# Kernel tuning notes

Hardware: AMD Instinct MI355X
Metric: run time of the kernel (lower is better)

Reference implementation:

```python
import jax, jax.numpy as jnp
import numpy as np

N = 20000   # nodes
E = 320000  # edges (avg degree 16)
H = 4       # heads
C = 128     # per-head / output channels (concat=False -> mean over heads)
IN = 2      # init_channels (TSP coords)
NEG_SLOPE = 0.2


def setup_inputs() -> dict:
    key = jax.random.key(0)
    ks = jax.random.split(key, 32)
    s = 0.1
    def W(k, shape):
        return (jax.random.normal(k, shape, jnp.float32) * s)
    inp = {
        "x": jax.random.normal(ks[0], (N, IN), jnp.float32),
        "edge_index": jax.random.randint(ks[1], (2, E), 0, N, jnp.int32),
        "edge_attr": jax.random.uniform(ks[2], (E, 1), jnp.float32),
    }
    i = 3
    for b in range(2):  # two parallel GATBlocks
        inp[f"Wsrc{b}"]  = W(ks[i+0], (IN, H * C))
        inp[f"bsrc{b}"]  = jnp.zeros((H * C,), jnp.float32)
        inp[f"Wdst{b}"]  = W(ks[i+1], (IN, H * C))
        inp[f"bdst{b}"]  = jnp.zeros((H * C,), jnp.float32)
        inp[f"Wedge{b}"] = W(ks[i+2], (1, H * C))
        inp[f"att{b}"]   = W(ks[i+3], (H, C))
        inp[f"bias{b}"]  = jnp.zeros((C,), jnp.float32)
        inp[f"Wres{b}"]  = W(ks[i+4], (IN, C))  # SkipConnection projection (2 -> 128)
        i += 5
    inp["Wfuse"] = W(ks[i], (2 * C, C))
    inp["bfuse"] = jnp.zeros((C,), jnp.float32)
    return inp


def _gat_block(x, src, dst, ea, Wsrc, bsrc, Wdst, bdst, Wedge, att, bias, Wres):
    # GATv2Conv (concat=False) + ReLU + residual projection
    xs = (x @ Wsrc + bsrc).reshape(N, H, C)   # lin_l (source / message)
    xd = (x @ Wdst + bdst).reshape(N, H, C)   # lin_r (target)
    ee = (ea @ Wedge).reshape(-1, H, C)       # lin_edge
    e = jax.nn.leaky_relu(xs[src] + xd[dst] + ee, NEG_SLOPE)  # [Etot,H,C]
    logits = jnp.einsum('ehc,hc->eh', e, att)                 # [Etot,H]
    # segment softmax over incoming edges of each target node
    m = jax.ops.segment_max(logits, dst, num_segments=N)
    m = jnp.where(jnp.isfinite(m), m, 0.0)
    p = jnp.exp(logits - m[dst])
    denom = jax.ops.segment_sum(p, dst, num_segments=N)
    alpha = p / (denom[dst] + 1e-16)                          # [Etot,H]
    agg = jax.ops.segment_sum(xs[src] * alpha[:, :, None], dst, num_segments=N)
    out = agg.mean(axis=1) + bias                             # concat=False: mean heads
    return jax.nn.relu(out) + x @ Wres                        # ReLU then skip add


def reference(x, edge_index, edge_attr,
              Wsrc0, bsrc0, Wdst0, bdst0, Wedge0, att0, bias0, Wres0,
              Wsrc1, bsrc1, Wdst1, bdst1, Wedge1, att1, bias1, Wres1,
              Wfuse, bfuse):
    src, dst = edge_index[0], edge_index[1]
    # PyG default add_self_loops=True, fill_value='mean' for edge_attr
    loop = jnp.arange(N, dtype=src.dtype)
    src_a = jnp.concatenate([src, loop])
    dst_a = jnp.concatenate([dst, loop])
    mean_attr = jnp.mean(edge_attr, axis=0, keepdims=True)
    ea = jnp.concatenate([edge_attr, jnp.broadcast_to(mean_attr, (N, 1))], axis=0)

    h0 = _gat_block(x, src_a, dst_a, ea, Wsrc0, bsrc0, Wdst0, bdst0, Wedge0, att0, bias0, Wres0)
    h1 = _gat_block(x, src_a, dst_a, ea, Wsrc1, bsrc1, Wdst1, bdst1, Wedge1, att1, bias1, Wres1)
    xc = jnp.concatenate([h0, h1], axis=-1)       # [N, 2C]
    return jax.nn.relu(xc @ Wfuse + bfuse)        # [N, C]
```

## Files before the change

### kernel.cpp

```cpp
#include <hip/hip_runtime.h>

#define HH 4
#define CC 128
#define NPB 64

typedef __attribute__((ext_vector_type(8))) short short8v;
typedef __attribute__((ext_vector_type(4))) float f32x4;

static inline size_t roundup256(size_t x) { return (x + 255) & ~(size_t)255; }

static __device__ __forceinline__ unsigned short f2bf(float f) {
    unsigned int u = __float_as_uint(f);
    unsigned int r = (u + 0x7FFFu + ((u >> 16) & 1u)) >> 16;
    return (unsigned short)r;
}

__global__ __launch_bounds__(256) void prep_kernel(
    const int* __restrict__ ei, const float* __restrict__ eattr,
    float* __restrict__ meansum, float* __restrict__ Lin, int* __restrict__ cnt,
    const float* __restrict__ Wsrc0, const float* __restrict__ bsrc0,
    const float* __restrict__ Wdst0, const float* __restrict__ bdst0,
    const float* __restrict__ Wedge0, const float* __restrict__ att0,
    const float* __restrict__ Wsrc1, const float* __restrict__ bsrc1,
    const float* __restrict__ Wdst1, const float* __restrict__ bdst1,
    const float* __restrict__ Wedge1, const float* __restrict__ att1,
    const float* __restrict__ Wfuse,
    float* __restrict__ packed, unsigned short* __restrict__ pwB, int E)
{
    int tid = blockIdx.x * 256 + threadIdx.x;
    int lane = threadIdx.x & 63, wid = threadIdx.x >> 6;
    float s = 0.f;
    if (tid < E) {
        atomicAdd(&cnt[ei[E + tid]], 1);
        s = eattr[tid];
    }
    #pragma unroll
    for (int off = 32; off > 0; off >>= 1) s += __shfl_down(s, off, 64);
    __shared__ float wsum[4];
    if (lane == 0) wsum[wid] = s;
    __syncthreads();
    if (threadIdx.x == 0)
        atomicAdd(meansum, wsum[0] + wsum[1] + wsum[2] + wsum[3]);

    if (blockIdx.x < 4) {
        int b = tid >> 9;
        int hc = tid & 511;
        int c = hc & 127;
        int h = hc >> 7;
        int bh = b * 4 + h;
        const float* Ws = b ? Wsrc1 : Wsrc0;
        const float* bs = b ? bsrc1 : bsrc0;
        const float* Wd = b ? Wdst1 : Wdst0;
        const float* bd = b ? bdst1 : bdst0;
        const float* We = b ? Wedge1 : Wedge0;
        const float* at = b ? att1 : att0;
        float A = Ws[hc], B = Ws[512 + hc];
        float C = Wd[hc], D = Wd[512 + hc];
        float Ec = We[hc];
        float F = bs[hc] + bd[hc];
        float a = at[hc];
        float4* r = (float4*)(packed + ((size_t)(bh * 128 + c)) * 8);
        r[0] = make_float4(A, B, C, D);
        r[1] = make_float4(Ec, F, 0.4f * a, 0.f);
        float sa = 0.6f * a;
        float vals[6] = {sa * A, sa * B, sa * C, sa * D, sa * Ec, sa * F};
        #pragma unroll
        for (int k = 0; k < 6; ++k) {
            float v = vals[k];
            #pragma unroll
            for (int off = 32; off > 0; off >>= 1) v += __shfl_down(v, off, 64);
            vals[k] = v;
        }
        __shared__ float Ls[4][6];
        if (lane == 0) {
            #pragma unroll
            for (int k = 0; k < 6; ++k) Ls[wid][k] = vals[k];
        }
        __syncthreads();
        if (threadIdx.x < 12) {
            int w2 = threadIdx.x / 6;
            int k = threadIdx.x % 6;
            int bhg = blockIdx.x * 2 + w2;
            Lin[bhg * 6 + k] = Ls[w2 * 2][k] + Ls[w2 * 2 + 1][k];
        }
    }

    if (blockIdx.x < 16) {
        int ct = tid >> 9;
        int kc = (tid >> 6) & 7;
        int l  = tid & 63;
        int c = ct * 16 + (l & 15);
        int kb = kc * 32 + (l >> 4) * 8;
        unsigned short v[8];
        #pragma unroll
        for (int j = 0; j < 8; ++j)
            v[j] = f2bf(Wfuse[(kb + j) * CC + c]);
        unsigned short* dst = pwB + (size_t)tid * 8;
        #pragma unroll
        for (int j = 0; j < 8; ++j) dst[j] = v[j];
    }
}

__global__ __launch_bounds__(1024) void scan_kernel(const int* __restrict__ cnt,
                                                    int* __restrict__ rowptr,
                                                    int* __restrict__ cur, int N) {
    const int CH = 32;
    int t = threadIdx.x;
    int base = t * CH;
    int local[CH];
    int s = 0;
    #pragma unroll
    for (int i = 0; i < CH; ++i) {
        int idx = base + i;
        int v = (idx < N) ? cnt[idx] + 1 : 0;
        local[i] = s;
        s += v;
    }
    __shared__ int sums[1024];
    sums[t] = s;
    __syncthreads();
    for (int off = 1; off < 1024; off <<= 1) {
        int v = (t >= off) ? sums[t - off] : 0;
        __syncthreads();
        sums[t] += v;
        __syncthreads();
    }
    int excl = sums[t] - s;
    #pragma unroll
    for (int i = 0; i < CH; ++i) {
        int idx = base + i;
        if (idx < N) {
            int v = excl + local[i];
            rowptr[idx] = v;
            cur[idx] = v;
        }
    }
    if (t == 1023) rowptr[N] = excl + s;
}

__global__ __launch_bounds__(256) void scatter_kernel(
    const int* __restrict__ ei, const float* __restrict__ x,
    const float* __restrict__ eattr, const float* __restrict__ meansum,
    int* __restrict__ cur, float4* __restrict__ ed4, float* __restrict__ ea1,
    int N, int E) {
    int e = blockIdx.x * 256 + threadIdx.x;
    int Etot = E + N;
    if (e >= Etot) return;
    int src, dst;
    float ea;
    if (e < E) { src = ei[e]; dst = ei[E + e]; ea = eattr[e]; }
    else       { src = e - E; dst = src; ea = meansum[0] / (float)E; }
    int pos = atomicAdd(&cur[dst], 1);
    const float2* x2 = (const float2*)x;
    float2 xs = x2[src];
    float2 xd = x2[dst];
    ed4[pos] = make_float4(xs.x, xs.y, xd.x, xd.y);
    ea1[pos] = ea;
}

__global__ __launch_bounds__(256) void logits_kernel(
    const float4* __restrict__ ed4,
    const float* __restrict__ ea1,
    const float* __restrict__ Lin,
    const float4* __restrict__ pw,
    float* __restrict__ p8, int EtotPad, int nchunks)
{
    int blk = blockIdx.x;
    int bh = blk / nchunks;
    int chunk = blk - bh * nchunks;
    int t = threadIdx.x;
    int iA = chunk * 512 + t;
    int iB = iA + 256;
    float4 eA = ed4[iA], eB = ed4[iB];
    float aA = ea1[iA], aB = ea1[iB];

    const float4* wp = pw + (size_t)bh * 256;
    float a0 = 0.f, a1 = 0.f;
    #pragma unroll 8
    for (int c = 0; c < 128; ++c) {
        float4 w0 = wp[2 * c];
        float4 w1 = wp[2 * c + 1];
        float uA = fmaf(w0.x, eA.x,
                   fmaf(w0.y, eA.y,
                   fmaf(w0.z, eA.z,
                   fmaf(w0.w, eA.w,
                   fmaf(w1.x, aA, w1.y)))));
        float uB = fmaf(w0.x, eB.x,
                   fmaf(w0.y, eB.y,
                   fmaf(w0.z, eB.z,
                   fmaf(w0.w, eB.w,
                   fmaf(w1.x, aB, w1.y)))));
        a0 = fmaf(w1.z, __builtin_fabsf(uA), a0);
        a1 = fmaf(w1.z, __builtin_fabsf(uB), a1);
    }

    const float* Lp = Lin + bh * 6;
    float lgA = fmaf(Lp[0], eA.x, fmaf(Lp[1], eA.y, fmaf(Lp[2], eA.z,
                fmaf(Lp[3], eA.w, fmaf(Lp[4], aA, Lp[5]))))) + a0;
    float lgB = fmaf(Lp[0], eB.x, fmaf(Lp[1], eB.y, fmaf(Lp[2], eB.z,
                fmaf(Lp[3], eB.w, fmaf(Lp[4], aB, Lp[5]))))) + a1;
    float* plane = p8 + (size_t)bh * EtotPad;
    plane[iA] = __expf(lgA);
    plane[iB] = __expf(lgB);
}

__global__ __launch_bounds__(256) void nodeS_kernel(
    const int* __restrict__ rowptr, const float4* __restrict__ ed4,
    const float* __restrict__ p8, float* __restrict__ S, int N, int EtotPad)
{
    int t = threadIdx.x;
    int g = t >> 3, bh = t & 7;
    int n = blockIdx.x * 32 + g;
    if (n >= N) return;
    int beg = rowptr[n], end = rowptr[n + 1];
    const float* plane = p8 + (size_t)bh * EtotPad;
    float s0 = 0.f, s1 = 0.f, sb = 0.f;
    for (int i = beg; i < end; ++i) {
        float4 ed = ed4[i];
        float p = plane[i];
        s0 = fmaf(p, ed.x, s0);
        s1 = fmaf(p, ed.y, s1);
        sb += p;
    }
    float rin = 1.f / (sb + 1e-16f);
    float* Sp = S + (size_t)n * 24 + bh * 3;
    Sp[0] = s0 * rin;
    Sp[1] = s1 * rin;
    Sp[2] = sb * rin;
}

__global__ __launch_bounds__(512) void node_kernel(
    const float* __restrict__ x,
    const float* __restrict__ S,
    const float* __restrict__ Wsrc0, const float* __restrict__ bsrc0,
    const float* __restrict__ bias0, const float* __restrict__ Wres0,
    const float* __restrict__ Wsrc1, const float* __restrict__ bsrc1,
    const float* __restrict__ bias1, const float* __restrict__ Wres1,
    const unsigned short* __restrict__ pwB, const float* __restrict__ bfuse,
    float* __restrict__ out, int N)
{
    __shared__ __align__(16) unsigned short hb[NPB][264];
    int t = threadIdx.x;
    int c = t & (CC - 1);
    int quarter = t >> 7;
    int n0 = blockIdx.x * NPB;

    float w00[HH], w01[HH], wb0[HH], w10[HH], w11[HH], wb1[HH];
    #pragma unroll
    for (int h = 0; h < HH; ++h) {
        w00[h] = Wsrc0[h * CC + c];
        w01[h] = Wsrc0[512 + h * CC + c];
        wb0[h] = bsrc0[h * CC + c];
        w10[h] = Wsrc1[h * CC + c];
        w11[h] = Wsrc1[512 + h * CC + c];
        wb1[h] = bsrc1[h * CC + c];
    }
    float bi0 = bias0[c], bi1 = bias1[c];
    float r00 = Wres0[c], r01 = Wres0[CC + c];
    float r10 = Wres1[c], r11 = Wres1[CC + c];

    for (int ni = quarter; ni < NPB; ni += 4) {
        int n = n0 + ni;
        if (n < N) {
            float x0 = x[2 * n], x1 = x[2 * n + 1];
            const float4* Sp4 = (const float4*)(S + (size_t)n * 24);
            float4 q0 = Sp4[0], q1 = Sp4[1], q2 = Sp4[2];
            float4 q3 = Sp4[3], q4 = Sp4[4], q5 = Sp4[5];
            float h0v, h1v;
            {
                float s0[HH] = {q0.x, q0.w, q1.z, q2.y};
                float s1[HH] = {q0.y, q1.x, q1.w, q2.z};
                float sb[HH] = {q0.z, q1.y, q2.x, q2.w};
                float acc = 0.f;
                #pragma unroll
                for (int h = 0; h < HH; ++h)
                    acc += fmaf(w00[h], s0[h], fmaf(w01[h], s1[h], wb0[h] * sb[h]));
                float o = fmaxf(acc * 0.25f + bi0, 0.f);
                h0v = o + x0 * r00 + x1 * r01;
            }
            {
                float s0[HH] = {q3.x, q3.w, q4.z, q5.y};
                float s1[HH] = {q3.y, q4.x, q4.w, q5.z};
                float sb[HH] = {q3.z, q4.y, q5.x, q5.w};
                float acc = 0.f;
                #pragma unroll
                for (int h = 0; h < HH; ++h)
                    acc += fmaf(w10[h], s0[h], fmaf(w11[h], s1[h], wb1[h] * sb[h]));
                float o = fmaxf(acc * 0.25f + bi1, 0.f);
                h1v = o + x0 * r10 + x1 * r11;
            }
            hb[ni][c] = f2bf(h0v);
            hb[ni][CC + c] = f2bf(h1v);
        }
    }
    __syncthreads();

    int w = t >> 6;
    int l = t & 63;
    int nt = w & 3;
    int cthalf = w >> 2;
    int row = nt * 16 + (l & 15);

    short8v a[8];
    #pragma unroll
    for (int kc = 0; kc < 8; ++kc)
        a[kc] = *reinterpret_cast<const short8v*>(&hb[row][kc * 32 + (l >> 4) * 8]);

    const short8v* pB = reinterpret_cast<const short8v*>(pwB);
    #pragma unroll
    for (int ci = 0; ci < 4; ++ci) {
        int ct = cthalf * 4 + ci;
        f32x4 acc = {0.f, 0.f, 0.f, 0.f};
        #pragma unroll
        for (int kc = 0; kc < 8; ++kc) {
            short8v b = pB[(ct * 8 + kc) * 64 + l];
            acc = __builtin_amdgcn_mfma_f32_16x16x32_bf16(a[kc], b, acc, 0, 0, 0);
        }
        int ch = ct * 16 + (l & 15);
        float bi = bfuse[ch];
        #pragma unroll
        for (int j = 0; j < 4; ++j) {
            int n = n0 + nt * 16 + (l >> 4) * 4 + j;
            if (n < N) out[(size_t)n * CC + ch] = fmaxf(acc[j] + bi, 0.f);
        }
    }
}

extern "C" void kernel_launch(void* const* d_in, const int* in_sizes, int n_in,
                              void* d_out, int out_size, void* d_ws, size_t ws_size,
                              hipStream_t stream) {
    const float* x      = (const float*)d_in[0];
    const int*   ei     = (const int*)d_in[1];
    const float* eattr  = (const float*)d_in[2];
    const float* Wsrc0  = (const float*)d_in[3];
    const float* bsrc0  = (const float*)d_in[4];
    const float* Wdst0  = (const float*)d_in[5];
    const float* bdst0  = (const float*)d_in[6];
    const float* Wedge0 = (const float*)d_in[7];
    const float* att0   = (const float*)d_in[8];
    const float* bias0  = (const float*)d_in[9];
    const float* Wres0  = (const float*)d_in[10];
    const float* Wsrc1  = (const float*)d_in[11];
    const float* bsrc1  = (const float*)d_in[12];
    const float* Wdst1  = (const float*)d_in[13];
    const float* bdst1  = (const float*)d_in[14];
    const float* Wedge1 = (const float*)d_in[15];
    const float* att1   = (const float*)d_in[16];
    const float* bias1  = (const float*)d_in[17];
    const float* Wres1  = (const float*)d_in[18];
    const float* Wfuse  = (const float*)d_in[19];
    const float* bfuse  = (const float*)d_in[20];
    float* out = (float*)d_out;

    int N = in_sizes[0] / 2;
    int E = in_sizes[1] / 2;
    int Etot = E + N;
    int EtotPad = (Etot + 511) & ~511;

    size_t off = 0;
    float* meansum = (float*)((char*)d_ws + off);  off += 256;
    int*   cnt     = (int*)((char*)d_ws + off);    off += roundup256((size_t)N * sizeof(int));
    size_t zero_bytes = off;
    float* Lin     = (float*)((char*)d_ws + off);  off += 256;
    int*   cur     = (int*)((char*)d_ws + off);    off += roundup256((size_t)N * sizeof(int));
    int*   rowptr  = (int*)((char*)d_ws + off);    off += roundup256((size_t)(N + 1) * sizeof(int));
    float* packed  = (float*)((char*)d_ws + off);  off += roundup256(8 * 128 * 8 * sizeof(float));
    unsigned short* pwB = (unsigned short*)((char*)d_ws + off);
                                                   off += roundup256(8 * 8 * 64 * 8 * sizeof(unsigned short));
    float4* ed4    = (float4*)((char*)d_ws + off); off += roundup256((size_t)EtotPad * sizeof(float4));
    float* ea1     = (float*)((char*)d_ws + off);  off += roundup256((size_t)EtotPad * sizeof(float));
    float* p8      = (float*)((char*)d_ws + off);  off += roundup256((size_t)EtotPad * 8 * sizeof(float));
    float* S       = (float*)((char*)d_ws + off);  off += roundup256((size_t)24 * N * sizeof(float));

    hipMemsetAsync(d_ws, 0, zero_bytes, stream);

    prep_kernel<<<(E + 255) / 256, 256, 0, stream>>>(
        ei, eattr, meansum, Lin, cnt,
        Wsrc0, bsrc0, Wdst0, bdst0, Wedge0, att0,
        Wsrc1, bsrc1, Wdst1, bdst1, Wedge1, att1,
        Wfuse, packed, pwB, E);

    scan_kernel<<<1, 1024, 0, stream>>>(cnt, rowptr, cur, N);

    scatter_kernel<<<(Etot + 255) / 256, 256, 0, stream>>>(
        ei, x, eattr, meansum, cur, ed4, ea1, N, E);

    int nchunks = EtotPad / 512;
    logits_kernel<<<8 * nchunks, 256, 0, stream>>>(
        ed4, ea1, Lin, (const float4*)packed, p8, EtotPad, nchunks);

    nodeS_kernel<<<(N + 31) / 32, 256, 0, stream>>>(rowptr, ed4, p8, S, N, EtotPad);

    node_kernel<<<(N + NPB - 1) / NPB, 512, 0, stream>>>(
        x, S,
        Wsrc0, bsrc0, bias0, Wres0,
        Wsrc1, bsrc1, bias1, Wres1,
        pwB, bfuse, out, N);
}
```

Baseline: 170.0 us.

## Compute GATv2 edge logits with bf16 MFMA instead of scalar FMA loops

The per-edge, per-channel pre-activation (a linear map of source/target coords, edge attribute and bias) is now a bf16 MFMA 16x16x32 product. Edge features form the A fragment and packed per-head weights form the B fragment. The abs-weighted reduction over channels uses cross-lane shuffles, and each block handles all 8 block-heads for 256 edges instead of one head per block. This targets the scalar FMA cost of the logits kernel. It adds bf16 rounding of the coordinates and weights, which may shift attention logits slightly.

```diff
diff --git a/kernel.cpp b/kernel.cpp
--- a/kernel.cpp
+++ b/kernel.cpp
@@ -17,7 +17,8 @@
 
 __global__ __launch_bounds__(256) void prep_kernel(
     const int* __restrict__ ei, const float* __restrict__ eattr,
-    float* __restrict__ meansum, float* __restrict__ Lin, int* __restrict__ cnt,
+    float* __restrict__ meansum, float* __restrict__ Lin,
+    float* __restrict__ gtab, int* __restrict__ cnt,
     const float* __restrict__ Wsrc0, const float* __restrict__ bsrc0,
     const float* __restrict__ Wdst0, const float* __restrict__ bdst0,
     const float* __restrict__ Wedge0, const float* __restrict__ att0,
@@ -25,7 +26,7 @@
     const float* __restrict__ Wdst1, const float* __restrict__ bdst1,
     const float* __restrict__ Wedge1, const float* __restrict__ att1,
     const float* __restrict__ Wfuse,
-    float* __restrict__ packed, unsigned short* __restrict__ pwB, int E)
+    unsigned short* __restrict__ pwL, unsigned short* __restrict__ pwB, int E)
 {
     int tid = blockIdx.x * 256 + threadIdx.x;
     int lane = threadIdx.x & 63, wid = threadIdx.x >> 6;
@@ -59,9 +60,7 @@
         float Ec = We[hc];
         float F = bs[hc] + bd[hc];
         float a = at[hc];
-        float4* r = (float4*)(packed + ((size_t)(bh * 128 + c)) * 8);
-        r[0] = make_float4(A, B, C, D);
-        r[1] = make_float4(Ec, F, 0.4f * a, 0.f);
+        gtab[bh * 128 + c] = 0.4f * a;
         float sa = 0.6f * a;
         float vals[6] = {sa * A, sa * B, sa * C, sa * D, sa * Ec, sa * F};
         #pragma unroll
@@ -85,17 +84,45 @@
         }
     }
 
-    if (blockIdx.x < 16) {
-        int ct = tid >> 9;
-        int kc = (tid >> 6) & 7;
-        int l  = tid & 63;
+    if (blockIdx.x >= 4 && blockIdx.x < 20) {
+        int t2 = tid - 1024;
+        int ct = t2 >> 9;
+        int kc = (t2 >> 6) & 7;
+        int l  = t2 & 63;
         int c = ct * 16 + (l & 15);
         int kb = kc * 32 + (l >> 4) * 8;
         unsigned short v[8];
         #pragma unroll
         for (int j = 0; j < 8; ++j)
             v[j] = f2bf(Wfuse[(kb + j) * CC + c]);
-        unsigned short* dst = pwB + (size_t)tid * 8;
+        unsigned short* dst = pwB + (size_t)t2 * 8;
+        #pragma unroll
+        for (int j = 0; j < 8; ++j) dst[j] = v[j];
+    }
+
+    if (blockIdx.x >= 20 && blockIdx.x < 36) {
+        int t2 = tid - 5120;
+        int bh = t2 >> 9;
+        int ct = (t2 >> 6) & 7;
+        int l  = t2 & 63;
+        unsigned short v[8] = {0, 0, 0, 0, 0, 0, 0, 0};
+        if (l < 16) {
+            int b = bh >> 2, h = bh & 3;
+            int c = ct * 16 + l;
+            int hc = h * 128 + c;
+            const float* Ws = b ? Wsrc1 : Wsrc0;
+            const float* bs = b ? bsrc1 : bsrc0;
+            const float* Wd = b ? Wdst1 : Wdst0;
+            const float* bd = b ? bdst1 : bdst0;
+            const float* We = b ? Wedge1 : Wedge0;
+            v[0] = f2bf(Ws[hc]);
+            v[1] = f2bf(Ws[512 + hc]);
+            v[2] = f2bf(Wd[hc]);
+            v[3] = f2bf(Wd[512 + hc]);
+            v[4] = f2bf(We[hc]);
+            v[5] = f2bf(bs[hc] + bd[hc]);
+        }
+        unsigned short* dst = pwL + (size_t)t2 * 8;
         #pragma unroll
         for (int j = 0; j < 8; ++j) dst[j] = v[j];
     }
@@ -162,46 +189,80 @@
     const float4* __restrict__ ed4,
     const float* __restrict__ ea1,
     const float* __restrict__ Lin,
-    const float4* __restrict__ pw,
-    float* __restrict__ p8, int EtotPad, int nchunks)
+    const float* __restrict__ gtab,
+    const unsigned short* __restrict__ pwL,
+    float* __restrict__ p8, int EtotPad)
 {
-    int blk = blockIdx.x;
-    int bh = blk / nchunks;
-    int chunk = blk - bh * nchunks;
     int t = threadIdx.x;
-    int iA = chunk * 512 + t;
-    int iB = iA + 256;
-    float4 eA = ed4[iA], eB = ed4[iB];
-    float aA = ea1[iA], aB = ea1[iB];
-
-    const float4* wp = pw + (size_t)bh * 256;
-    float a0 = 0.f, a1 = 0.f;
-    #pragma unroll 8
-    for (int c = 0; c < 128; ++c) {
-        float4 w0 = wp[2 * c];
-        float4 w1 = wp[2 * c + 1];
-        float uA = fmaf(w0.x, eA.x,
-                   fmaf(w0.y, eA.y,
-                   fmaf(w0.z, eA.z,
-                   fmaf(w0.w, eA.w,
-                   fmaf(w1.x, aA, w1.y)))));
-        float uB = fmaf(w0.x, eB.x,
-                   fmaf(w0.y, eB.y,
-                   fmaf(w0.z, eB.z,
-                   fmaf(w0.w, eB.w,
-                   fmaf(w1.x, aB, w1.y)))));
-        a0 = fmaf(w1.z, __builtin_fabsf(uA), a0);
-        a1 = fmaf(w1.z, __builtin_fabsf(uB), a1);
-    }
-
-    const float* Lp = Lin + bh * 6;
-    float lgA = fmaf(Lp[0], eA.x, fmaf(Lp[1], eA.y, fmaf(Lp[2], eA.z,
-                fmaf(Lp[3], eA.w, fmaf(Lp[4], aA, Lp[5]))))) + a0;
-    float lgB = fmaf(Lp[0], eB.x, fmaf(Lp[1], eB.y, fmaf(Lp[2], eB.z,
-                fmaf(Lp[3], eB.w, fmaf(Lp[4], aB, Lp[5]))))) + a1;
-    float* plane = p8 + (size_t)bh * EtotPad;
-    plane[iA] = __expf(lgA);
-    plane[iB] = __expf(lgB);
+    int w = t >> 6, l = t & 63;
+    int base = blockIdx.x * 256 + w * 64;
+    int col = l & 15, grp = l >> 4;
+
+    short8v a[4];
+    #pragma unroll
+    for (int et = 0; et < 4; ++et) {
+        short8v v = {0, 0, 0, 0, 0, 0, 0, 0};
+        if (grp == 0) {
+            int e = base + et * 16 + col;
+            float4 ev = ed4[e];
+            float ea = ea1[e];
+            v[0] = (short)f2bf(ev.x);
+            v[1] = (short)f2bf(ev.y);
+            v[2] = (short)f2bf(ev.z);
+            v[3] = (short)f2bf(ev.w);
+            v[4] = (short)f2bf(ea);
+            v[5] = (short)f2bf(1.0f);
+        }
+        a[et] = v;
+    }
+
+    const short8v* pB = reinterpret_cast<const short8v*>(pwL);
+
+    #pragma unroll
+    for (int bh = 0; bh < 8; ++bh) {
+        f32x4 acc[4];
+        #pragma unroll
+        for (int et = 0; et < 4; ++et) acc[et] = (f32x4){0.f, 0.f, 0.f, 0.f};
+
+        #pragma unroll
+        for (int ct = 0; ct < 8; ++ct) {
+            short8v bfrag = pB[(bh * 8 + ct) * 64 + l];
+            float g = gtab[bh * 128 + ct * 16 + col];
+            #pragma unroll
+            for (int et = 0; et < 4; ++et) {
+                f32x4 u = __builtin_amdgcn_mfma_f32_16x16x32_bf16(
+                    a[et], bfrag, (f32x4){0.f, 0.f, 0.f, 0.f}, 0, 0, 0);
+                #pragma unroll
+                for (int j = 0; j < 4; ++j)
+                    acc[et][j] = fmaf(g, __builtin_fabsf(u[j]), acc[et][j]);
+            }
+        }
+
+        const float* Lp = Lin + bh * 6;
+        float l0 = Lp[0], l1 = Lp[1], l2 = Lp[2], l3 = Lp[3], l4 = Lp[4], l5 = Lp[5];
+        float* plane = p8 + (size_t)bh * EtotPad;
+
+        #pragma unroll
+        for (int et = 0; et < 4; ++et) {
+            float s0 = acc[et][0], s1 = acc[et][1], s2 = acc[et][2], s3 = acc[et][3];
+            #pragma unroll
+            for (int m = 1; m < 16; m <<= 1) {
+                s0 += __shfl_xor(s0, m);
+                s1 += __shfl_xor(s1, m);
+                s2 += __shfl_xor(s2, m);
+                s3 += __shfl_xor(s3, m);
+            }
+            if (col < 4) {
+                float sv = (col == 0) ? s0 : (col == 1) ? s1 : (col == 2) ? s2 : s3;
+                int e = base + et * 16 + grp * 4 + col;
+                float4 ev = ed4[e];
+                float ea = ea1[e];
+                float lg = fmaf(l0, ev.x, fmaf(l1, ev.y, fmaf(l2, ev.z,
+                           fmaf(l3, ev.w, fmaf(l4, ea, l5))))) + sv;
+                plane[e] = __expf(lg);
+            }
+        }
+    }
 }
 
 __global__ __launch_bounds__(256) void nodeS_kernel(
@@ -362,11 +423,13 @@
     int*   cnt     = (int*)((char*)d_ws + off);    off += roundup256((size_t)N * sizeof(int));
     size_t zero_bytes = off;
     float* Lin     = (float*)((char*)d_ws + off);  off += 256;
+    float* gtab    = (float*)((char*)d_ws + off);  off += roundup256(1024 * sizeof(float));
     int*   cur     = (int*)((char*)d_ws + off);    off += roundup256((size_t)N * sizeof(int));
     int*   rowptr  = (int*)((char*)d_ws + off);    off += roundup256((size_t)(N + 1) * sizeof(int));
-    float* packed  = (float*)((char*)d_ws + off);  off += roundup256(8 * 128 * 8 * sizeof(float));
     unsigned short* pwB = (unsigned short*)((char*)d_ws + off);
-                                                   off += roundup256(8 * 8 * 64 * 8 * sizeof(unsigned short));
+                                                   off += roundup256(4096 * 8 * sizeof(unsigned short));
+    unsigned short* pwL = (unsigned short*)((char*)d_ws + off);
+                                                   off += roundup256(4096 * 8 * sizeof(unsigned short));
     float4* ed4    = (float4*)((char*)d_ws + off); off += roundup256((size_t)EtotPad * sizeof(float4));
     float* ea1     = (float*)((char*)d_ws + off);  off += roundup256((size_t)EtotPad * sizeof(float));
     float* p8      = (float*)((char*)d_ws + off);  off += roundup256((size_t)EtotPad * 8 * sizeof(float));
@@ -375,19 +438,18 @@
     hipMemsetAsync(d_ws, 0, zero_bytes, stream);
 
     prep_kernel<<<(E + 255) / 256, 256, 0, stream>>>(
-        ei, eattr, meansum, Lin, cnt,
+        ei, eattr, meansum, Lin, gtab, cnt,
         Wsrc0, bsrc0, Wdst0, bdst0, Wedge0, att0,
         Wsrc1, bsrc1, Wdst1, bdst1, Wedge1, att1,
-        Wfuse, packed, pwB, E);
+        Wfuse, pwL, pwB, E);
 
     scan_kernel<<<1, 1024, 0, stream>>>(cnt, rowptr, cur, N);
 
     scatter_kernel<<<(Etot + 255) / 256, 256, 0, stream>>>(
         ei, x, eattr, meansum, cur, ed4, ea1, N, E);
 
-    int nchunks = EtotPad / 512;
-    logits_kernel<<<8 * nchunks, 256, 0, stream>>>(
-        ed4, ea1, Lin, (const float4*)packed, p8, EtotPad, nchunks);
+    logits_kernel<<<EtotPad / 256, 256, 0, stream>>>(
+        ed4, ea1, Lin, gtab, pwL, p8, EtotPad);
 
     nodeS_kernel<<<(N + 31) / 32, 256, 0, stream>>>(rowptr, ed4, p8, S, N, EtotPad);
 
```

Result: slower. 198.7 us (+16.9%).

## Fuse per-node softmax aggregation into node kernel via shared memory

Applied to the files above, without the earlier changes.

Removes the separate nodeS kernel and computes the per-node normalized attention sums inside node_kernel, keeping them in shared memory instead of writing and rereading a global S buffer. The scatter kernel now also stores the source index per CSR slot, and the aggregation gathers x[src] through it rather than reading the 16-byte ed4 records. It also moves the Wfuse bf16 packing to prep blocks 4–19 so it no longer shares blocks 0–3 with other prep work. The cost is an extra esrc write and random gathers into x, plus a longer, possibly imbalanced prologue in node_kernel before its barrier.

```diff
diff --git a/kernel.cpp b/kernel.cpp
--- a/kernel.cpp
+++ b/kernel.cpp
@@ -85,17 +85,18 @@
         }
     }
 
-    if (blockIdx.x < 16) {
-        int ct = tid >> 9;
-        int kc = (tid >> 6) & 7;
-        int l  = tid & 63;
+    if (blockIdx.x >= 4 && blockIdx.x < 20) {
+        int t2 = tid - 1024;
+        int ct = t2 >> 9;
+        int kc = (t2 >> 6) & 7;
+        int l  = t2 & 63;
         int c = ct * 16 + (l & 15);
         int kb = kc * 32 + (l >> 4) * 8;
         unsigned short v[8];
         #pragma unroll
         for (int j = 0; j < 8; ++j)
             v[j] = f2bf(Wfuse[(kb + j) * CC + c]);
-        unsigned short* dst = pwB + (size_t)tid * 8;
+        unsigned short* dst = pwB + (size_t)t2 * 8;
         #pragma unroll
         for (int j = 0; j < 8; ++j) dst[j] = v[j];
     }
@@ -142,7 +143,7 @@
     const int* __restrict__ ei, const float* __restrict__ x,
     const float* __restrict__ eattr, const float* __restrict__ meansum,
     int* __restrict__ cur, float4* __restrict__ ed4, float* __restrict__ ea1,
-    int N, int E) {
+    int* __restrict__ esrc, int N, int E) {
     int e = blockIdx.x * 256 + threadIdx.x;
     int Etot = E + N;
     if (e >= Etot) return;
@@ -156,6 +157,7 @@
     float2 xd = x2[dst];
     ed4[pos] = make_float4(xs.x, xs.y, xd.x, xd.y);
     ea1[pos] = ea;
+    esrc[pos] = src;
 }
 
 __global__ __launch_bounds__(256) void logits_kernel(
@@ -204,46 +206,49 @@
     plane[iB] = __expf(lgB);
 }
 
-__global__ __launch_bounds__(256) void nodeS_kernel(
-    const int* __restrict__ rowptr, const float4* __restrict__ ed4,
-    const float* __restrict__ p8, float* __restrict__ S, int N, int EtotPad)
-{
-    int t = threadIdx.x;
-    int g = t >> 3, bh = t & 7;
-    int n = blockIdx.x * 32 + g;
-    if (n >= N) return;
-    int beg = rowptr[n], end = rowptr[n + 1];
-    const float* plane = p8 + (size_t)bh * EtotPad;
-    float s0 = 0.f, s1 = 0.f, sb = 0.f;
-    for (int i = beg; i < end; ++i) {
-        float4 ed = ed4[i];
-        float p = plane[i];
-        s0 = fmaf(p, ed.x, s0);
-        s1 = fmaf(p, ed.y, s1);
-        sb += p;
-    }
-    float rin = 1.f / (sb + 1e-16f);
-    float* Sp = S + (size_t)n * 24 + bh * 3;
-    Sp[0] = s0 * rin;
-    Sp[1] = s1 * rin;
-    Sp[2] = sb * rin;
-}
-
 __global__ __launch_bounds__(512) void node_kernel(
     const float* __restrict__ x,
-    const float* __restrict__ S,
+    const int* __restrict__ rowptr,
+    const int* __restrict__ esrc,
+    const float* __restrict__ p8,
     const float* __restrict__ Wsrc0, const float* __restrict__ bsrc0,
     const float* __restrict__ bias0, const float* __restrict__ Wres0,
     const float* __restrict__ Wsrc1, const float* __restrict__ bsrc1,
     const float* __restrict__ bias1, const float* __restrict__ Wres1,
     const unsigned short* __restrict__ pwB, const float* __restrict__ bfuse,
-    float* __restrict__ out, int N)
+    float* __restrict__ out, int N, int EtotPad)
 {
     __shared__ __align__(16) unsigned short hb[NPB][264];
+    __shared__ __align__(16) float Sl[NPB][24];
     int t = threadIdx.x;
+    int n0 = blockIdx.x * NPB;
+    const float2* x2 = (const float2*)x;
+
+    {
+        int g = t >> 3, bh = t & 7;
+        int n = n0 + g;
+        if (n < N) {
+            int beg = rowptr[n], end = rowptr[n + 1];
+            const float* plane = p8 + (size_t)bh * EtotPad;
+            float s0 = 0.f, s1 = 0.f, sb = 0.f;
+            for (int i = beg; i < end; ++i) {
+                float p = plane[i];
+                int srcu = esrc[i];
+                float2 xs = x2[srcu];
+                s0 = fmaf(p, xs.x, s0);
+                s1 = fmaf(p, xs.y, s1);
+                sb += p;
+            }
+            float rin = 1.f / (sb + 1e-16f);
+            Sl[g][bh * 3 + 0] = s0 * rin;
+            Sl[g][bh * 3 + 1] = s1 * rin;
+            Sl[g][bh * 3 + 2] = sb * rin;
+        }
+    }
+    __syncthreads();
+
     int c = t & (CC - 1);
     int quarter = t >> 7;
-    int n0 = blockIdx.x * NPB;
 
     float w00[HH], w01[HH], wb0[HH], w10[HH], w11[HH], wb1[HH];
     #pragma unroll
@@ -263,7 +268,7 @@
         int n = n0 + ni;
         if (n < N) {
             float x0 = x[2 * n], x1 = x[2 * n + 1];
-            const float4* Sp4 = (const float4*)(S + (size_t)n * 24);
+            const float4* Sp4 = (const float4*)&Sl[ni][0];
             float4 q0 = Sp4[0], q1 = Sp4[1], q2 = Sp4[2];
             float4 q3 = Sp4[3], q4 = Sp4[4], q5 = Sp4[5];
             float h0v, h1v;
@@ -366,11 +371,11 @@
     int*   rowptr  = (int*)((char*)d_ws + off);    off += roundup256((size_t)(N + 1) * sizeof(int));
     float* packed  = (float*)((char*)d_ws + off);  off += roundup256(8 * 128 * 8 * sizeof(float));
     unsigned short* pwB = (unsigned short*)((char*)d_ws + off);
-                                                   off += roundup256(8 * 8 * 64 * 8 * sizeof(unsigned short));
+                                                   off += roundup256(4096 * 8 * sizeof(unsigned short));
     float4* ed4    = (float4*)((char*)d_ws + off); off += roundup256((size_t)EtotPad * sizeof(float4));
     float* ea1     = (float*)((char*)d_ws + off);  off += roundup256((size_t)EtotPad * sizeof(float));
+    int*   esrc    = (int*)((char*)d_ws + off);    off += roundup256((size_t)EtotPad * sizeof(int));
     float* p8      = (float*)((char*)d_ws + off);  off += roundup256((size_t)EtotPad * 8 * sizeof(float));
-    float* S       = (float*)((char*)d_ws + off);  off += roundup256((size_t)24 * N * sizeof(float));
 
     hipMemsetAsync(d_ws, 0, zero_bytes, stream);
 
@@ -383,17 +388,15 @@
     scan_kernel<<<1, 1024, 0, stream>>>(cnt, rowptr, cur, N);
 
     scatter_kernel<<<(Etot + 255) / 256, 256, 0, stream>>>(
-        ei, x, eattr, meansum, cur, ed4, ea1, N, E);
+        ei, x, eattr, meansum, cur, ed4, ea1, esrc, N, E);
 
     int nchunks = EtotPad / 512;
     logits_kernel<<<8 * nchunks, 256, 0, stream>>>(
         ed4, ea1, Lin, (const float4*)packed, p8, EtotPad, nchunks);
 
-    nodeS_kernel<<<(N + 31) / 32, 256, 0, stream>>>(rowptr, ed4, p8, S, N, EtotPad);
-
     node_kernel<<<(N + NPB - 1) / NPB, 512, 0, stream>>>(
-        x, S,
+        x, rowptr, esrc, p8,
         Wsrc0, bsrc0, bias0, Wres0,
         Wsrc1, bsrc1, bias1, Wres1,
-        pwB, bfuse, out, N);
-}
+        pwB, bfuse, out, N, EtotPad);
+}
```

After: 162.6 us. -4.3%, faster.
